# Performance work log

Measured on AMD Instinct MI355X. Metric: run time of the kernel, lower is better.

The kernel has to match this reference:

```python
import jax, jax.numpy as jnp
import numpy as np


def _layer_norm(x, w, b, eps=1e-5):
    mu = jnp.mean(x, axis=-1, keepdims=True)
    xc = x - mu
    var = jnp.mean(xc * xc, axis=-1, keepdims=True)
    return xc * jax.lax.rsqrt(var + eps) * w + b


def setup_inputs() -> dict:
    key = jax.random.key(0)
    ks = jax.random.split(key, 6)
    S, B, H = 2048, 2, 1024
    NH, NKV, HD = 16, 4, 64
    E, K, F = 8, 2, 4096
    w = lambda k, shape: 0.02 * jax.random.normal(k, shape, dtype=jnp.float32)
    return {
        "hidden_states": jax.random.normal(ks[0], (S, B, H), dtype=jnp.float32),
        "ln1_weight": jnp.ones((H,), jnp.float32),
        "ln1_bias": jnp.zeros((H,), jnp.float32),
        "ln2_weight": jnp.ones((H,), jnp.float32),
        "ln2_bias": jnp.zeros((H,), jnp.float32),
        "qkv_weight": w(ks[1], (H, (NH + 2 * NKV) * HD)),
        "proj_weight": w(ks[2], (H, H)),
        "router_weight": w(ks[3], (H, E)),
        "moe_w1": w(ks[4], (E, H, F)),
        "moe_w2": w(ks[5], (E, F, H)),
        "num_heads": NH,
        "num_kv_heads": NKV,
        "top_k": K,
    }


def reference(hidden_states, ln1_weight, ln1_bias, ln2_weight, ln2_bias,
              qkv_weight, proj_weight, router_weight, moe_w1, moe_w2,
              num_heads, num_kv_heads, top_k):
    S, B, H = hidden_states.shape
    HD = H // num_heads
    scale = 1.0 / (HD ** 0.5)

    # --- LN1 -> QKV projection (GQA split) ---
    ln1 = _layer_norm(hidden_states, ln1_weight, ln1_bias)
    qkv = ln1 @ qkv_weight                               # [S,B,(NH+2NKV)*HD]
    q_end = num_heads * HD
    k_end = q_end + num_kv_heads * HD
    q = qkv[..., :q_end].reshape(S, B, num_heads, HD)
    k = qkv[..., q_end:k_end].reshape(S, B, num_kv_heads, HD)
    v = qkv[..., k_end:].reshape(S, B, num_kv_heads, HD)
    rep = num_heads // num_kv_heads                      # repeat_interleave on head dim
    k = jnp.repeat(k, rep, axis=2)
    v = jnp.repeat(v, rep, axis=2)

    # --- causal SDPA, layout [B,NH,S,HD] ---
    q_bf = q.transpose(1, 2, 0, 3)
    k_bf = k.transpose(1, 2, 0, 3)
    v_bf = v.transpose(1, 2, 0, 3)
    scores = jnp.einsum('bhqd,bhkd->bhqk', q_bf, k_bf) * scale
    causal = jnp.tril(jnp.ones((S, S), dtype=bool))
    scores = jnp.where(causal, scores, jnp.finfo(scores.dtype).min)
    p = jax.nn.softmax(scores, axis=-1)
    attn = jnp.einsum('bhqk,bhkd->bhqd', p, v_bf)
    attn_out = attn.transpose(2, 0, 1, 3).reshape(S, B, H)  # back to [S,B,H]

    # --- output projection + residual ---
    h_attn = hidden_states + attn_out @ proj_weight

    # --- LN2 -> router top-k -> expert FFN -> weighted combine ---
    ln2 = _layer_norm(h_attn, ln2_weight, ln2_bias)
    T = S * B
    x = ln2.reshape(T, H)
    logits = x @ router_weight                           # [T,E]
    probs = jax.nn.softmax(logits, axis=-1)
    top_p, top_i = jax.lax.top_k(probs, top_k)           # [T,K]

    def expert_fn(_, w):
        w1, w2 = w
        return None, jax.nn.gelu(x @ w1, approximate=False) @ w2  # [T,H]

    _, outs = jax.lax.scan(expert_fn, None, (moe_w1, moe_w2))     # [E,T,H]
    gathered = outs[top_i, jnp.arange(T)[:, None], :]             # [T,K,H]
    moe_out = jnp.sum(gathered * top_p[..., None].astype(outs.dtype), axis=1)

    return h_attn + moe_out.reshape(S, B, H)
```

## Files before the change

### kernel.cpp

```cpp
#include <hip/hip_runtime.h>
#include <hip/hip_bf16.h>

constexpr int TT   = 4096;
constexpr int HH   = 1024;
constexpr int QKVN = 1536;
constexpr int FF   = 4096;

using f16x8  = __attribute__((ext_vector_type(8))) _Float16;
using f16x4  = __attribute__((ext_vector_type(4))) _Float16;
using bf16x8 = __attribute__((ext_vector_type(8))) short;
using s16x4  = __attribute__((ext_vector_type(4))) short;
using f32x4  = __attribute__((ext_vector_type(4))) float;

static __device__ __forceinline__ f32x4 mfma16(f16x8 a, f16x8 b, f32x4 c) {
  return __builtin_amdgcn_mfma_f32_16x16x32_f16(a, b, c, 0, 0, 0);
}
static __device__ __forceinline__ f32x4 mfmabf(bf16x8 a, bf16x8 b, f32x4 c) {
  return __builtin_amdgcn_mfma_f32_16x16x32_bf16(a, b, c, 0, 0, 0);
}
static __device__ __forceinline__ short f2bf(float f) {
  union { float f; unsigned u; } v; v.f = f;
  unsigned r = v.u + 0x7fffu + ((v.u >> 16) & 1u);
  return (short)(r >> 16);
}
static __device__ __forceinline__ void split16(float f, _Float16 &h, _Float16 &l) {
  _Float16 hh = (_Float16)f; h = hh; l = (_Float16)(f - (float)hh);
}
static __device__ __forceinline__ float fast_gelu(float x) {
  float u = 0.7978845608f * (x + 0.044715f * x * x * x);
  float a = __expf(-2.0f * fabsf(u));
  float t = (1.0f - a) * __builtin_amdgcn_rcpf(1.0f + a);
  t = copysignf(t, u);
  return 0.5f * x * (1.0f + t);
}
static __device__ __forceinline__ void gload16(const void* g, void* l) {
  __builtin_amdgcn_global_load_lds((__attribute__((address_space(1))) void*)(g),
                                   (__attribute__((address_space(3))) void*)(l), 16, 0, 0);
}

__global__ void zero_cnt(int* cnt) { if (threadIdx.x < 8) cnt[threadIdx.x] = 0; }

__global__ __launch_bounds__(256) void wconv_split(const float* __restrict__ W,
    _Float16* __restrict__ oh, _Float16* __restrict__ ol, int K, int N)
{
  __shared__ float ts[64][68];
  int n0 = blockIdx.x * 64, k0 = blockIdx.y * 64, t = threadIdx.x;
  #pragma unroll
  for (int it = 0; it < 4; it++) {
    int el = it * 1024 + t * 4; int r = el >> 6, c = el & 63;
    float4 v = *(const float4*)&W[(size_t)(k0 + r) * N + n0 + c];
    *(float4*)&ts[r][c] = v;
  }
  __syncthreads();
  #pragma unroll
  for (int it = 0; it < 4; it++) {
    int el = it * 1024 + t * 4; int nr = el >> 6, kc = el & 63;
    f16x4 hv, lv;
    #pragma unroll
    for (int q = 0; q < 4; q++) { _Float16 hh, ll; split16(ts[kc + q][nr], hh, ll); hv[q] = hh; lv[q] = ll; }
    size_t o = (size_t)(n0 + nr) * K + k0 + kc;
    *(f16x4*)&oh[o] = hv; *(f16x4*)&ol[o] = lv;
  }
}

__global__ __launch_bounds__(256) void wconv_bf(const float* __restrict__ W,
    short* __restrict__ o, int K, int N)
{
  __shared__ float ts[64][68];
  const float* Wz = W + (size_t)blockIdx.z * K * N;
  short* oz = o + (size_t)blockIdx.z * K * N;
  int n0 = blockIdx.x * 64, k0 = blockIdx.y * 64, t = threadIdx.x;
  #pragma unroll
  for (int it = 0; it < 4; it++) {
    int el = it * 1024 + t * 4; int r = el >> 6, c = el & 63;
    float4 v = *(const float4*)&Wz[(size_t)(k0 + r) * N + n0 + c];
    *(float4*)&ts[r][c] = v;
  }
  __syncthreads();
  #pragma unroll
  for (int it = 0; it < 4; it++) {
    int el = it * 1024 + t * 4; int nr = el >> 6, kc = el & 63;
    s16x4 bv;
    #pragma unroll
    for (int q = 0; q < 4; q++) bv[q] = f2bf(ts[kc + q][nr]);
    *(s16x4*)&oz[(size_t)(n0 + nr) * K + k0 + kc] = bv;
  }
}

__global__ __launch_bounds__(256) void vtrans(const float* __restrict__ qkv,
    _Float16* __restrict__ vh, _Float16* __restrict__ vl)
{
  __shared__ float ts[64][68];
  int bkv = blockIdx.x, b = bkv >> 2, kvh = bkv & 3;
  int s0 = blockIdx.y * 64, t = threadIdx.x;
  #pragma unroll
  for (int it = 0; it < 4; it++) {
    int el = it * 1024 + t * 4; int r = el >> 6, c = el & 63;
    float4 v = *(const float4*)&qkv[(size_t)((s0 + r) * 2 + b) * QKVN + 1280 + kvh * 64 + c];
    *(float4*)&ts[r][c] = v;
  }
  __syncthreads();
  #pragma unroll
  for (int it = 0; it < 4; it++) {
    int el = it * 1024 + t * 4; int d = el >> 6, sc = el & 63;
    f16x4 hv, lv;
    #pragma unroll
    for (int q = 0; q < 4; q++) { _Float16 hh, ll; split16(ts[sc + q][d], hh, ll); hv[q] = hh; lv[q] = ll; }
    size_t o = ((size_t)bkv * 64 + d) * 2048 + s0 + sc;
    *(f16x4*)&vh[o] = hv; *(f16x4*)&vl[o] = lv;
  }
}

template<int MODE>
__global__ __launch_bounds__(256) void ln_split(const float* __restrict__ in,
    const float* __restrict__ wt, const float* __restrict__ bs,
    _Float16* __restrict__ oh, _Float16* __restrict__ ol,
    float* __restrict__ xo, short* __restrict__ xbo)
{
  int row = blockIdx.x, tid = threadIdx.x;
  const float4* ip = (const float4*)(in + (size_t)row * HH);
  float4 v = ip[tid];
  float s = v.x + v.y + v.z + v.w;
  #pragma unroll
  for (int m = 1; m < 64; m <<= 1) s += __shfl_xor(s, m, 64);
  __shared__ float red1[4], red2[4];
  int wid = tid >> 6;
  if ((tid & 63) == 0) red1[wid] = s;
  __syncthreads();
  float mu = (red1[0] + red1[1] + red1[2] + red1[3]) * (1.0f / HH);
  float4 c; c.x = v.x - mu; c.y = v.y - mu; c.z = v.z - mu; c.w = v.w - mu;
  float s2 = c.x*c.x + c.y*c.y + c.z*c.z + c.w*c.w;
  #pragma unroll
  for (int m = 1; m < 64; m <<= 1) s2 += __shfl_xor(s2, m, 64);
  if ((tid & 63) == 0) red2[wid] = s2;
  __syncthreads();
  float ve = (red2[0] + red2[1] + red2[2] + red2[3]) * (1.0f / HH) + 1e-5f;
  float rs = rsqrtf(ve);
  rs = rs * (1.5f - 0.5f * ve * rs * rs);
  float4 wv = ((const float4*)wt)[tid], bv = ((const float4*)bs)[tid];
  float o4[4];
  o4[0] = c.x * rs * wv.x + bv.x; o4[1] = c.y * rs * wv.y + bv.y;
  o4[2] = c.z * rs * wv.z + bv.z; o4[3] = c.w * rs * wv.w + bv.w;
  size_t base = (size_t)row * HH + tid * 4;
  if (MODE == 0) {
    f16x4 hv, lv;
    #pragma unroll
    for (int q = 0; q < 4; q++) { _Float16 hh, ll; split16(o4[q], hh, ll); hv[q] = hh; lv[q] = ll; }
    *(f16x4*)&oh[base] = hv; *(f16x4*)&ol[base] = lv;
  } else {
    float4 ov; ov.x = o4[0]; ov.y = o4[1]; ov.z = o4[2]; ov.w = o4[3];
    *(float4*)&xo[base] = ov;
    s16x4 bvv;
    #pragma unroll
    for (int q = 0; q < 4; q++) bvv[q] = f2bf(o4[q]);
    *(s16x4*)&xbo[base] = bvv;
  }
}

template<int EPI>
__global__ __launch_bounds__(256) void gemm_split2(
    const _Float16* __restrict__ Agh, const _Float16* __restrict__ Agl,
    const _Float16* __restrict__ Bgh, const _Float16* __restrict__ Bgl,
    int K, float* __restrict__ C, int ldc, const float* __restrict__ resid,
    _Float16* __restrict__ kh, _Float16* __restrict__ kl)
{
  __shared__ _Float16 AhS[4096], AlS[4096], BhS[4096], BlS[4096];
  const int tid = threadIdx.x, lane = tid & 63, w = tid >> 6;
  const int wr = w >> 1, wc = w & 1;
  const int m0 = blockIdx.y * 128, n0 = blockIdx.x * 128;
  f32x4 acc[4][4] = {};
  const _Float16 *pah[2], *pal[2], *pbh[2], *pbl[2];
  int ldsb[2];
  #pragma unroll
  for (int i = 0; i < 2; i++) {
    int E = i * 2048 + w * 512 + lane * 8;
    int r = E >> 5, cc = E & 31;
    int cs = cc ^ ((r & 3) << 3);
    pah[i] = Agh + (size_t)(m0 + r) * K + cs;
    pal[i] = Agl + (size_t)(m0 + r) * K + cs;
    pbh[i] = Bgh + (size_t)(n0 + r) * K + cs;
    pbl[i] = Bgl + (size_t)(n0 + r) * K + cs;
    ldsb[i] = i * 2048 + w * 512;
  }
  const int rr = lane & 15, ko = (lane >> 4) * 8;
  const int xo = (rr & 3) << 3;
  for (int k0 = 0; k0 < K; k0 += 32) {
    __syncthreads();
    #pragma unroll
    for (int i = 0; i < 2; i++) {
      gload16(pah[i] + k0, &AhS[ldsb[i]]);
      gload16(pal[i] + k0, &AlS[ldsb[i]]);
      gload16(pbh[i] + k0, &BhS[ldsb[i]]);
      gload16(pbl[i] + k0, &BlS[ldsb[i]]);
    }
    __syncthreads();
    f16x8 fah[4], fal[4], fbh[4], fbl[4];
    #pragma unroll
    for (int m = 0; m < 4; m++) {
      int ro = (wr * 64 + m * 16 + rr) * 32 + (ko ^ xo);
      fah[m] = *(const f16x8*)&AhS[ro];
      fal[m] = *(const f16x8*)&AlS[ro];
    }
    #pragma unroll
    for (int n = 0; n < 4; n++) {
      int ro = (wc * 64 + n * 16 + rr) * 32 + (ko ^ xo);
      fbh[n] = *(const f16x8*)&BhS[ro];
      fbl[n] = *(const f16x8*)&BlS[ro];
    }
    #pragma unroll
    for (int m = 0; m < 4; m++)
      #pragma unroll
      for (int n = 0; n < 4; n++) {
        acc[m][n] = mfma16(fah[m], fbh[n], acc[m][n]);
        acc[m][n] = mfma16(fah[m], fbl[n], acc[m][n]);
        acc[m][n] = mfma16(fal[m], fbh[n], acc[m][n]);
      }
  }
  int r0 = m0 + wr * 64 + (lane >> 4) * 4;
  int c0 = n0 + wc * 64 + (lane & 15);
  #pragma unroll
  for (int m = 0; m < 4; m++)
    #pragma unroll
    for (int n = 0; n < 4; n++)
      #pragma unroll
      for (int j = 0; j < 4; j++) {
        int tr = r0 + m * 16 + j, tc = c0 + n * 16;
        size_t idx = (size_t)tr * ldc + tc;
        float v = acc[m][n][j];
        if (EPI == 1) v += resid[idx];
        C[idx] = v;
        if (EPI == 0 && tc >= 1024 && tc < 1280) {
          int s = tr >> 1, bb = tr & 1;
          int kvh = (tc - 1024) >> 6, d = (tc - 1024) & 63;
          _Float16 hh, ll; split16(v, hh, ll);
          size_t kidx = ((size_t)(bb * 4 + kvh) * 2048 + s) * 64 + d;
          kh[kidx] = hh; kl[kidx] = ll;
        }
      }
}

__global__ __launch_bounds__(256) void attn2(const float* __restrict__ qkv,
    const _Float16* __restrict__ khg, const _Float16* __restrict__ klg,
    const _Float16* __restrict__ vhg, const _Float16* __restrict__ vlg,
    _Float16* __restrict__ aoh, _Float16* __restrict__ aol)
{
  __shared__ _Float16 KhS[4096], KlS[4096], VhS[4096], VlS[4096];
  __shared__ _Float16 Ph[64][72], Pl[64][72];
  int bh = blockIdx.x;
  int qt = gridDim.y - 1 - blockIdx.y;
  int h = bh >> 1, b = bh & 1, kvh = h >> 2, bkv = b * 4 + kvh;
  int q0 = qt * 64;
  int tid = threadIdx.x, lane = tid & 63, w = tid >> 6;
  int rr = lane & 15, ko = (lane >> 4) * 8;
  const int xo8 = (rr & 7) << 3;
  int qrow = q0 + w * 16 + rr;
  const float* qp = qkv + (size_t)(qrow * 2 + b) * QKVN + h * 64;
  f16x8 qh[2], ql[2];
  #pragma unroll
  for (int kk = 0; kk < 2; kk++) {
    const float4* p = (const float4*)(qp + kk * 32 + ko);
    float4 v0 = p[0], v1 = p[1];
    float tq[8] = {v0.x, v0.y, v0.z, v0.w, v1.x, v1.y, v1.z, v1.w};
    f16x8 hv, lv;
    #pragma unroll
    for (int q = 0; q < 8; q++) { _Float16 hh, ll; split16(tq[q], hh, ll); hv[q] = hh; lv[q] = ll; }
    qh[kk] = hv; ql[kk] = lv;
  }
  const _Float16 *pk[2][2], *pv[2][2];
  int ldsb[2];
  #pragma unroll
  for (int i = 0; i < 2; i++) {
    int E = i * 2048 + w * 512 + lane * 8;
    int r = E >> 6, cc = E & 63;
    int cs = cc ^ ((r & 7) << 3);
    pk[i][0] = khg + ((size_t)bkv * 2048 + r) * 64 + cs;
    pk[i][1] = klg + ((size_t)bkv * 2048 + r) * 64 + cs;
    pv[i][0] = vhg + ((size_t)bkv * 64 + r) * 2048 + cs;
    pv[i][1] = vlg + ((size_t)bkv * 64 + r) * 2048 + cs;
    ldsb[i] = i * 2048 + w * 512;
  }
  f32x4 o[4] = {};
  float mo[4] = {-1e30f, -1e30f, -1e30f, -1e30f};
  float lo[4] = {0.f, 0.f, 0.f, 0.f};
  for (int ks = 0; ks <= q0; ks += 64) {
    __syncthreads();
    #pragma unroll
    for (int i = 0; i < 2; i++) {
      gload16(pk[i][0] + (size_t)ks * 64, &KhS[ldsb[i]]);
      gload16(pk[i][1] + (size_t)ks * 64, &KlS[ldsb[i]]);
      gload16(pv[i][0] + ks, &VhS[ldsb[i]]);
      gload16(pv[i][1] + ks, &VlS[ldsb[i]]);
    }
    __syncthreads();
    f32x4 s[4] = {};
    __builtin_amdgcn_s_setprio(1);
    #pragma unroll
    for (int n = 0; n < 4; n++)
      #pragma unroll
      for (int kk = 0; kk < 2; kk++) {
        int ro = (n * 16 + rr) * 64 + ((kk * 32 + ko) ^ xo8);
        f16x8 kbh = *(const f16x8*)&KhS[ro];
        f16x8 kbl = *(const f16x8*)&KlS[ro];
        s[n] = mfma16(qh[kk], kbh, s[n]);
        s[n] = mfma16(qh[kk], kbl, s[n]);
        s[n] = mfma16(ql[kk], kbh, s[n]);
      }
    __builtin_amdgcn_s_setprio(0);
    bool diag = (ks == q0);
    int myrow = q0 + w * 16 + (lane >> 4) * 4;
    #pragma unroll
    for (int n = 0; n < 4; n++)
      #pragma unroll
      for (int j = 0; j < 4; j++) {
        float v = s[n][j] * 0.125f;
        if (diag && (ks + n * 16 + rr) > (myrow + j)) v = -1e30f;
        s[n][j] = v;
      }
    float mt[4];
    #pragma unroll
    for (int j = 0; j < 4; j++) mt[j] = fmaxf(fmaxf(s[0][j], s[1][j]), fmaxf(s[2][j], s[3][j]));
    #pragma unroll
    for (int msk = 1; msk < 16; msk <<= 1)
      #pragma unroll
      for (int j = 0; j < 4; j++) mt[j] = fmaxf(mt[j], __shfl_xor(mt[j], msk, 64));
    float pvv[4][4], rsum[4];
    #pragma unroll
    for (int j = 0; j < 4; j++) {
      float mn = fmaxf(mo[j], mt[j]);
      float al = expf(mo[j] - mn);
      mo[j] = mn;
      rsum[j] = 0.f;
      #pragma unroll
      for (int n = 0; n < 4; n++) { float pp = expf(s[n][j] - mn); pvv[n][j] = pp; rsum[j] += pp; }
      lo[j] *= al;
      #pragma unroll
      for (int n = 0; n < 4; n++) o[n][j] *= al;
    }
    #pragma unroll
    for (int msk = 1; msk < 16; msk <<= 1)
      #pragma unroll
      for (int j = 0; j < 4; j++) rsum[j] += __shfl_xor(rsum[j], msk, 64);
    #pragma unroll
    for (int j = 0; j < 4; j++) lo[j] += rsum[j];
    int prow = w * 16 + (lane >> 4) * 4;
    #pragma unroll
    for (int n = 0; n < 4; n++)
      #pragma unroll
      for (int j = 0; j < 4; j++) {
        _Float16 hh, ll; split16(pvv[n][j], hh, ll);
        Ph[prow + j][n * 16 + rr] = hh;
        Pl[prow + j][n * 16 + rr] = ll;
      }
    __builtin_amdgcn_s_setprio(1);
    #pragma unroll
    for (int kk = 0; kk < 2; kk++) {
      f16x8 pah = *(const f16x8*)&Ph[w * 16 + rr][kk * 32 + ko];
      f16x8 pal = *(const f16x8*)&Pl[w * 16 + rr][kk * 32 + ko];
      #pragma unroll
      for (int dn = 0; dn < 4; dn++) {
        int ro = (dn * 16 + rr) * 64 + ((kk * 32 + ko) ^ xo8);
        f16x8 vbh = *(const f16x8*)&VhS[ro];
        f16x8 vbl = *(const f16x8*)&VlS[ro];
        o[dn] = mfma16(pah, vbh, o[dn]);
        o[dn] = mfma16(pah, vbl, o[dn]);
        o[dn] = mfma16(pal, vbh, o[dn]);
      }
    }
    __builtin_amdgcn_s_setprio(0);
  }
  float inv[4];
  #pragma unroll
  for (int j = 0; j < 4; j++) inv[j] = 1.0f / lo[j];
  int orow = q0 + w * 16 + (lane >> 4) * 4;
  int ocol = h * 64 + rr;
  #pragma unroll
  for (int dn = 0; dn < 4; dn++)
    #pragma unroll
    for (int j = 0; j < 4; j++) {
      float v = o[dn][j] * inv[j];
      _Float16 hh, ll; split16(v, hh, ll);
      size_t idx = (size_t)((orow + j) * 2 + b) * HH + ocol + dn * 16;
      aoh[idx] = hh; aol[idx] = ll;
    }
}

__global__ __launch_bounds__(256) void router_kernel(const float* __restrict__ x,
    const float* __restrict__ rw, int* __restrict__ list, float* __restrict__ listp,
    int* __restrict__ cnt)
{
  __shared__ float rws[HH * 8];
  int tid = threadIdx.x;
  for (int i = tid; i < HH * 8; i += 256) rws[i] = rw[i];
  __syncthreads();
  int t = blockIdx.x * 4 + (tid >> 6);
  int lane = tid & 63;
  const float* xp = x + (size_t)t * HH;
  float acc[8] = {};
  for (int i = lane; i < HH; i += 64) {
    float xv = xp[i];
    #pragma unroll
    for (int e = 0; e < 8; e++) acc[e] += xv * rws[i * 8 + e];
  }
  #pragma unroll
  for (int e = 0; e < 8; e++)
    #pragma unroll
    for (int m = 1; m < 64; m <<= 1) acc[e] += __shfl_xor(acc[e], m, 64);
  if (lane == 0) {
    float mx = acc[0];
    #pragma unroll
    for (int e = 1; e < 8; e++) mx = fmaxf(mx, acc[e]);
    float p[8], sum = 0.f;
    #pragma unroll
    for (int e = 0; e < 8; e++) { p[e] = expf(acc[e] - mx); sum += p[e]; }
    float inv = 1.0f / sum;
    int i1 = 0; float v1 = acc[0];
    #pragma unroll
    for (int e = 1; e < 8; e++) if (acc[e] > v1) { v1 = acc[e]; i1 = e; }
    int i2 = -1; float v2 = -3.4e38f;
    #pragma unroll
    for (int e = 0; e < 8; e++) if (e != i1 && acc[e] > v2) { v2 = acc[e]; i2 = e; }
    int pos1 = atomicAdd(&cnt[i1], 1);
    list[i1 * TT + pos1] = t; listp[i1 * TT + pos1] = p[i1] * inv;
    int pos2 = atomicAdd(&cnt[i2], 1);
    list[i2 * TT + pos2] = t; listp[i2 * TT + pos2] = p[i2] * inv;
  }
}

__global__ __launch_bounds__(256) void moe1_full(const short* __restrict__ xbf,
    const short* __restrict__ w1T, const int* __restrict__ list,
    const int* __restrict__ cnt, short* __restrict__ hidden)
{
  int e = blockIdx.z;
  int ce = cnt[e];
  int off = 0;
  #pragma unroll
  for (int i = 0; i < 8; i++) if (i < e) off += cnt[i];
  int m0 = blockIdx.y * 128;
  if (m0 >= ce) return;
  int n0 = blockIdx.x * 128;
  __shared__ short AS[8192], BS[8192];
  const int tid = threadIdx.x, lane = tid & 63, w = tid >> 6;
  const int wr = w >> 1, wc = w & 1;
  f32x4 acc[4][4] = {};
  const short *pa[4], *pb[4];
  int ldsb[4];
  #pragma unroll
  for (int i = 0; i < 4; i++) {
    int E = i * 2048 + w * 512 + lane * 8;
    int r = E >> 6, c = E & 63;
    int cs = c ^ ((r & 7) << 3);
    int apos = m0 + r; if (apos > ce - 1) apos = ce - 1;
    int tok = list[e * TT + apos];
    pa[i] = xbf + (size_t)tok * HH + cs;
    pb[i] = w1T + ((size_t)e * FF + n0 + r) * HH + cs;
    ldsb[i] = E;
  }
  const int rr = lane & 15, ko = (lane >> 4) * 8;
  const int xo = (rr & 7) << 3;
  for (int k0 = 0; k0 < HH; k0 += 64) {
    __syncthreads();
    #pragma unroll
    for (int i = 0; i < 4; i++) {
      gload16(pa[i] + k0, &AS[ldsb[i]]);
      gload16(pb[i] + k0, &BS[ldsb[i]]);
    }
    __syncthreads();
    #pragma unroll
    for (int kk = 0; kk < 2; kk++) {
      bf16x8 fa[4], fb[4];
      #pragma unroll
      for (int m = 0; m < 4; m++) fa[m] = *(const bf16x8*)&AS[(wr * 64 + m * 16 + rr) * 64 + ((kk * 32 + ko) ^ xo)];
      #pragma unroll
      for (int n = 0; n < 4; n++) fb[n] = *(const bf16x8*)&BS[(wc * 64 + n * 16 + rr) * 64 + ((kk * 32 + ko) ^ xo)];
      #pragma unroll
      for (int m = 0; m < 4; m++)
        #pragma unroll
        for (int n = 0; n < 4; n++) acc[m][n] = mfmabf(fa[m], fb[n], acc[m][n]);
    }
  }
  int p0 = m0 + wr * 64 + (lane >> 4) * 4;
  int c0 = n0 + wc * 64 + (lane & 15);
  #pragma unroll
  for (int m = 0; m < 4; m++)
    #pragma unroll
    for (int n = 0; n < 4; n++)
      #pragma unroll
      for (int j = 0; j < 4; j++) {
        int pos = p0 + m * 16 + j;
        if (pos < ce) {
          float v = fast_gelu(acc[m][n][j]);
          hidden[(size_t)(off + pos) * FF + c0 + n * 16] = f2bf(v);
        }
      }
}

__global__ __launch_bounds__(256) void moe2_full(const short* __restrict__ hidden,
    const short* __restrict__ w2T, const int* __restrict__ list,
    const float* __restrict__ listp, const int* __restrict__ cnt,
    float* __restrict__ outp)
{
  int e = blockIdx.z;
  int ce = cnt[e];
  int off = 0;
  #pragma unroll
  for (int i = 0; i < 8; i++) if (i < e) off += cnt[i];
  int m0 = blockIdx.y * 128;
  if (m0 >= ce) return;
  int n0 = blockIdx.x * 128;
  __shared__ short AS[8192], BS[8192];
  const int tid = threadIdx.x, lane = tid & 63, w = tid >> 6;
  const int wr = w >> 1, wc = w & 1;
  f32x4 acc[4][4] = {};
  const short *pa[4], *pb[4];
  int ldsb[4];
  #pragma unroll
  for (int i = 0; i < 4; i++) {
    int E = i * 2048 + w * 512 + lane * 8;
    int r = E >> 6, c = E & 63;
    int cs = c ^ ((r & 7) << 3);
    int apos = m0 + r; if (apos > ce - 1) apos = ce - 1;
    pa[i] = hidden + ((size_t)off + apos) * FF + cs;
    pb[i] = w2T + ((size_t)e * HH + n0 + r) * FF + cs;
    ldsb[i] = E;
  }
  const int rr = lane & 15, ko = (lane >> 4) * 8;
  const int xo = (rr & 7) << 3;
  for (int k0 = 0; k0 < FF; k0 += 64) {
    __syncthreads();
    #pragma unroll
    for (int i = 0; i < 4; i++) {
      gload16(pa[i] + k0, &AS[ldsb[i]]);
      gload16(pb[i] + k0, &BS[ldsb[i]]);
    }
    __syncthreads();
    #pragma unroll
    for (int kk = 0; kk < 2; kk++) {
      bf16x8 fa[4], fb[4];
      #pragma unroll
      for (int m = 0; m < 4; m++) fa[m] = *(const bf16x8*)&AS[(wr * 64 + m * 16 + rr) * 64 + ((kk * 32 + ko) ^ xo)];
      #pragma unroll
      for (int n = 0; n < 4; n++) fb[n] = *(const bf16x8*)&BS[(wc * 64 + n * 16 + rr) * 64 + ((kk * 32 + ko) ^ xo)];
      #pragma unroll
      for (int m = 0; m < 4; m++)
        #pragma unroll
        for (int n = 0; n < 4; n++) acc[m][n] = mfmabf(fa[m], fb[n], acc[m][n]);
    }
  }
  int p0 = m0 + wr * 64 + (lane >> 4) * 4;
  int c0 = n0 + wc * 64 + (lane & 15);
  #pragma unroll
  for (int m = 0; m < 4; m++)
    #pragma unroll
    for (int j = 0; j < 4; j++) {
      int pos = p0 + m * 16 + j;
      if (pos < ce) {
        int tk = list[e * TT + pos];
        float pw = listp[e * TT + pos];
        #pragma unroll
        for (int n = 0; n < 4; n++)
          atomicAdd(&outp[(size_t)tk * HH + c0 + n * 16], pw * acc[m][n][j]);
      }
    }
}

__global__ __launch_bounds__(256) void moe_gemm1(const float* __restrict__ x,
    const float* __restrict__ w1, const int* __restrict__ list,
    const int* __restrict__ cnt, short* __restrict__ hidden, int e)
{
  int ce = cnt[e];
  int m0 = blockIdx.y * 128;
  if (m0 >= ce) return;
  int n0 = blockIdx.x * 128;
  __shared__ short As[128][40], Bs[128][40];
  int tid = threadIdx.x, lane = tid & 63, w = tid >> 6, wr = w >> 1, wc = w & 1;
  f32x4 acc[4][4] = {};
  int arow = tid >> 1, akh = (tid & 1) * 16;
  int apos = m0 + arow;
  int tok = list[(size_t)e * TT + (apos < ce ? apos : 0)];
  const float* ap = x + (size_t)tok * HH + akh;
  int bn = tid & 127, bkh = (tid >> 7) * 16;
  const float* bp = w1 + (size_t)e * HH * FF + (size_t)bkh * FF + n0 + bn;
  for (int k0 = 0; k0 < HH; k0 += 32) {
    __syncthreads();
    {
      const float4* p = (const float4*)(ap + k0);
      bf16x8 s0, s1;
      #pragma unroll
      for (int q = 0; q < 2; q++) { float4 v = p[q]; s0[q*4] = f2bf(v.x); s0[q*4+1] = f2bf(v.y); s0[q*4+2] = f2bf(v.z); s0[q*4+3] = f2bf(v.w); }
      #pragma unroll
      for (int q = 0; q < 2; q++) { float4 v = p[q+2]; s1[q*4] = f2bf(v.x); s1[q*4+1] = f2bf(v.y); s1[q*4+2] = f2bf(v.z); s1[q*4+3] = f2bf(v.w); }
      *(bf16x8*)&As[arow][akh] = s0; *(bf16x8*)&As[arow][akh+8] = s1;
    }
    {
      const float* p = bp + (size_t)k0 * FF;
      bf16x8 s0, s1;
      #pragma unroll
      for (int q = 0; q < 8; q++) s0[q] = f2bf(p[(size_t)q * FF]);
      #pragma unroll
      for (int q = 0; q < 8; q++) s1[q] = f2bf(p[(size_t)(q+8) * FF]);
      *(bf16x8*)&Bs[bn][bkh] = s0; *(bf16x8*)&Bs[bn][bkh+8] = s1;
    }
    __syncthreads();
    int rr = lane & 15, ko = (lane >> 4) * 8;
    bf16x8 fa[4], fb[4];
    #pragma unroll
    for (int m = 0; m < 4; m++) fa[m] = *(bf16x8*)&As[wr*64 + m*16 + rr][ko];
    #pragma unroll
    for (int n = 0; n < 4; n++) fb[n] = *(bf16x8*)&Bs[wc*64 + n*16 + rr][ko];
    #pragma unroll
    for (int m = 0; m < 4; m++)
      #pragma unroll
      for (int n = 0; n < 4; n++) acc[m][n] = mfmabf(fa[m], fb[n], acc[m][n]);
  }
  int p0 = m0 + wr*64 + (lane >> 4) * 4;
  int c0 = n0 + wc*64 + (lane & 15);
  #pragma unroll
  for (int m = 0; m < 4; m++)
    #pragma unroll
    for (int n = 0; n < 4; n++)
      #pragma unroll
      for (int j = 0; j < 4; j++) {
        int pos = p0 + m*16 + j;
        if (pos < ce) {
          float v = acc[m][n][j];
          v = 0.5f * v * (1.0f + erff(v * 0.70710678f));
          hidden[(size_t)pos * FF + c0 + n*16] = f2bf(v);
        }
      }
}

__global__ __launch_bounds__(256) void moe_gemm2(const short* __restrict__ hidden,
    const float* __restrict__ w2, const int* __restrict__ list,
    const float* __restrict__ listp, const int* __restrict__ cnt,
    float* __restrict__ outp, int e)
{
  int ce = cnt[e];
  int m0 = blockIdx.y * 128;
  if (m0 >= ce) return;
  int n0 = blockIdx.x * 128;
  __shared__ short As[128][40], Bs[128][40];
  int tid = threadIdx.x, lane = tid & 63, w = tid >> 6, wr = w >> 1, wc = w & 1;
  f32x4 acc[4][4] = {};
  int arow = tid >> 1, akh = (tid & 1) * 16;
  int apos = m0 + arow;
  const short* ap = hidden + (size_t)(apos < ce ? apos : 0) * FF + akh;
  int bn = tid & 127, bkh = (tid >> 7) * 16;
  const float* bp = w2 + (size_t)e * FF * HH + (size_t)bkh * HH + n0 + bn;
  for (int k0 = 0; k0 < FF; k0 += 32) {
    __syncthreads();
    {
      const int4* p = (const int4*)(ap + k0);
      int4 a0 = p[0], a1 = p[1];
      *(int4*)&As[arow][akh]   = a0;
      *(int4*)&As[arow][akh+8] = a1;
    }
    {
      const float* p = bp + (size_t)k0 * HH;
      bf16x8 s0, s1;
      #pragma unroll
      for (int q = 0; q < 8; q++) s0[q] = f2bf(p[(size_t)q * HH]);
      #pragma unroll
      for (int q = 0; q < 8; q++) s1[q] = f2bf(p[(size_t)(q+8) * HH]);
      *(bf16x8*)&Bs[bn][bkh] = s0; *(bf16x8*)&Bs[bn][bkh+8] = s1;
    }
    __syncthreads();
    int rr = lane & 15, ko = (lane >> 4) * 8;
    bf16x8 fa[4], fb[4];
    #pragma unroll
    for (int m = 0; m < 4; m++) fa[m] = *(bf16x8*)&As[wr*64 + m*16 + rr][ko];
    #pragma unroll
    for (int n = 0; n < 4; n++) fb[n] = *(bf16x8*)&Bs[wc*64 + n*16 + rr][ko];
    #pragma unroll
    for (int m = 0; m < 4; m++)
      #pragma unroll
      for (int n = 0; n < 4; n++) acc[m][n] = mfmabf(fa[m], fb[n], acc[m][n]);
  }
  int p0 = m0 + wr*64 + (lane >> 4) * 4;
  int c0 = n0 + wc*64 + (lane & 15);
  #pragma unroll
  for (int m = 0; m < 4; m++)
    #pragma unroll
    for (int j = 0; j < 4; j++) {
      int pos = p0 + m*16 + j;
      if (pos < ce) {
        int tk = list[(size_t)e * TT + pos];
        float pw = listp[(size_t)e * TT + pos];
        #pragma unroll
        for (int n = 0; n < 4; n++)
          atomicAdd(&outp[(size_t)tk * HH + c0 + n*16], pw * acc[m][n][j]);
      }
    }
}

extern "C" void kernel_launch(void* const* d_in, const int* in_sizes, int n_in,
                              void* d_out, int out_size, void* d_ws, size_t ws_size,
                              hipStream_t stream)
{
  const float* hs      = (const float*)d_in[0];
  const float* ln1w    = (const float*)d_in[1];
  const float* ln1b    = (const float*)d_in[2];
  const float* ln2w    = (const float*)d_in[3];
  const float* ln2b    = (const float*)d_in[4];
  const float* qkvw    = (const float*)d_in[5];
  const float* projw   = (const float*)d_in[6];
  const float* routerw = (const float*)d_in[7];
  const float* w1      = (const float*)d_in[8];
  const float* w2      = (const float*)d_in[9];
  float* out = (float*)d_out;

  const size_t MB = 1024 * 1024;
  char* wsb = (char*)d_ws;
  bool full = ws_size >= 153 * MB;

  float*    qkvbuf = (float*)wsb;
  _Float16* khb    = (_Float16*)(wsb + 24 * MB);
  _Float16* klb    = (_Float16*)(wsb + 26 * MB);
  _Float16* vhb    = (_Float16*)(wsb + 28 * MB);
  _Float16* vlb    = (_Float16*)(wsb + 30 * MB);
  short*    hidden = (short*)wsb;
  size_t r2 = full ? 64 * MB : 32 * MB;
  _Float16* ln1h = (_Float16*)(wsb + r2);
  _Float16* ln1l = (_Float16*)(wsb + r2 + 8 * MB);
  _Float16* aohb = ln1h;
  _Float16* aolb = ln1l;
  float*    xbuf = (float*)(wsb + r2);
  short*    xbf  = (short*)(wsb + r2 + 16 * MB);
  size_t r3 = full ? 88 * MB : 56 * MB;
  _Float16* qkvwTh  = (_Float16*)(wsb + r3);
  _Float16* qkvwTl  = (_Float16*)(wsb + r3 + 3 * MB);
  _Float16* projwTh = (_Float16*)(wsb + r3 + 6 * MB);
  _Float16* projwTl = (_Float16*)(wsb + r3 + 8 * MB);
  short*    w1T     = (short*)(wsb + r3);
  short*    w2T     = (short*)(wsb + r3);
  size_t r4 = full ? 152 * MB : 66 * MB;
  int*   list  = (int*)(wsb + r4);
  float* listp = (float*)(wsb + r4 + 128 * 1024);
  int*   cnt   = (int*)(wsb + r4 + 256 * 1024);

  zero_cnt<<<1, 64, 0, stream>>>(cnt);
  wconv_split<<<dim3(QKVN / 64, HH / 64), 256, 0, stream>>>(qkvw, qkvwTh, qkvwTl, HH, QKVN);
  wconv_split<<<dim3(HH / 64, HH / 64), 256, 0, stream>>>(projw, projwTh, projwTl, HH, HH);
  ln_split<0><<<TT, 256, 0, stream>>>(hs, ln1w, ln1b, ln1h, ln1l, nullptr, nullptr);
  gemm_split2<0><<<dim3(QKVN / 128, TT / 128), 256, 0, stream>>>(
      ln1h, ln1l, qkvwTh, qkvwTl, HH, qkvbuf, QKVN, nullptr, khb, klb);
  vtrans<<<dim3(8, 32), 256, 0, stream>>>(qkvbuf, vhb, vlb);
  attn2<<<dim3(32, 32), 256, 0, stream>>>(qkvbuf, khb, klb, vhb, vlb, aohb, aolb);
  gemm_split2<1><<<dim3(HH / 128, TT / 128), 256, 0, stream>>>(
      aohb, aolb, projwTh, projwTl, HH, out, HH, hs, nullptr, nullptr);
  ln_split<1><<<TT, 256, 0, stream>>>(out, ln2w, ln2b, nullptr, nullptr, xbuf, xbf);
  router_kernel<<<TT / 4, 256, 0, stream>>>(xbuf, routerw, list, listp, cnt);
  if (full) {
    wconv_bf<<<dim3(FF / 64, HH / 64, 8), 256, 0, stream>>>(w1, w1T, HH, FF);
    moe1_full<<<dim3(FF / 128, TT / 128, 8), 256, 0, stream>>>(xbf, w1T, list, cnt, hidden);
    wconv_bf<<<dim3(HH / 64, FF / 64, 8), 256, 0, stream>>>(w2, w2T, FF, HH);
    moe2_full<<<dim3(HH / 128, TT / 128, 8), 256, 0, stream>>>(hidden, w2T, list, listp, cnt, out);
  } else {
    for (int e = 0; e < 8; e++) {
      moe_gemm1<<<dim3(FF / 128, TT / 128), 256, 0, stream>>>(xbuf, w1, list, cnt, hidden, e);
      moe_gemm2<<<dim3(HH / 128, TT / 128), 256, 0, stream>>>(hidden, w2, list, listp, cnt, out, e);
    }
  }
}
```

Before: 699.0 us.

## Interleave expert blocks in 1D grid and double-buffer LDS in MoE down-projection

Both MoE GEMM kernels now use a flat 1D grid with the expert index in the low bits. This interleaves blocks from different experts and pushes the early-exit check ahead of the offset computation, so work is spread more evenly across CUs. The second MoE GEMM also gains double-buffered LDS tiles: it prefetches the next K-slice while running MFMAs on the current one, with one barrier per iteration and s_setprio around the compute. This doubles LDS use for that kernel, which may reduce occupancy.

```diff
diff --git a/kernel.cpp b/kernel.cpp
--- a/kernel.cpp
+++ b/kernel.cpp
@@ -430,14 +430,17 @@
     const short* __restrict__ w1T, const int* __restrict__ list,
     const int* __restrict__ cnt, short* __restrict__ hidden)
 {
-  int e = blockIdx.z;
+  int id = blockIdx.x;
+  int e = id & 7;
+  int inner = id >> 3;
+  int mx = inner & 31, nx = inner >> 5;
   int ce = cnt[e];
+  int m0 = mx * 128;
+  if (m0 >= ce) return;
+  int n0 = nx * 128;
   int off = 0;
   #pragma unroll
   for (int i = 0; i < 8; i++) if (i < e) off += cnt[i];
-  int m0 = blockIdx.y * 128;
-  if (m0 >= ce) return;
-  int n0 = blockIdx.x * 128;
   __shared__ short AS[8192], BS[8192];
   const int tid = threadIdx.x, lane = tid & 63, w = tid >> 6;
   const int wr = w >> 1, wc = w & 1;
@@ -499,15 +502,18 @@
     const float* __restrict__ listp, const int* __restrict__ cnt,
     float* __restrict__ outp)
 {
-  int e = blockIdx.z;
+  int id = blockIdx.x;
+  int e = id & 7;
+  int inner = id >> 3;
+  int mx = inner & 31, nx = inner >> 5;
   int ce = cnt[e];
+  int m0 = mx * 128;
+  if (m0 >= ce) return;
+  int n0 = nx * 128;
   int off = 0;
   #pragma unroll
   for (int i = 0; i < 8; i++) if (i < e) off += cnt[i];
-  int m0 = blockIdx.y * 128;
-  if (m0 >= ce) return;
-  int n0 = blockIdx.x * 128;
-  __shared__ short AS[8192], BS[8192];
+  __shared__ short AS[2][8192], BS[2][8192];
   const int tid = threadIdx.x, lane = tid & 63, w = tid >> 6;
   const int wr = w >> 1, wc = w & 1;
   f32x4 acc[4][4] = {};
@@ -525,26 +531,38 @@
   }
   const int rr = lane & 15, ko = (lane >> 4) * 8;
   const int xo = (rr & 7) << 3;
+  #pragma unroll
+  for (int i = 0; i < 4; i++) {
+    gload16(pa[i], &AS[0][ldsb[i]]);
+    gload16(pb[i], &BS[0][ldsb[i]]);
+  }
+  __syncthreads();
+  int cb = 0;
   for (int k0 = 0; k0 < FF; k0 += 64) {
-    __syncthreads();
-    #pragma unroll
-    for (int i = 0; i < 4; i++) {
-      gload16(pa[i] + k0, &AS[ldsb[i]]);
-      gload16(pb[i] + k0, &BS[ldsb[i]]);
-    }
-    __syncthreads();
+    int nk = k0 + 64;
+    if (nk < FF) {
+      #pragma unroll
+      for (int i = 0; i < 4; i++) {
+        gload16(pa[i] + nk, &AS[cb ^ 1][ldsb[i]]);
+        gload16(pb[i] + nk, &BS[cb ^ 1][ldsb[i]]);
+      }
+    }
+    __builtin_amdgcn_s_setprio(1);
     #pragma unroll
     for (int kk = 0; kk < 2; kk++) {
       bf16x8 fa[4], fb[4];
       #pragma unroll
-      for (int m = 0; m < 4; m++) fa[m] = *(const bf16x8*)&AS[(wr * 64 + m * 16 + rr) * 64 + ((kk * 32 + ko) ^ xo)];
-      #pragma unroll
-      for (int n = 0; n < 4; n++) fb[n] = *(const bf16x8*)&BS[(wc * 64 + n * 16 + rr) * 64 + ((kk * 32 + ko) ^ xo)];
+      for (int m = 0; m < 4; m++) fa[m] = *(const bf16x8*)&AS[cb][(wr * 64 + m * 16 + rr) * 64 + ((kk * 32 + ko) ^ xo)];
+      #pragma unroll
+      for (int n = 0; n < 4; n++) fb[n] = *(const bf16x8*)&BS[cb][(wc * 64 + n * 16 + rr) * 64 + ((kk * 32 + ko) ^ xo)];
       #pragma unroll
       for (int m = 0; m < 4; m++)
         #pragma unroll
         for (int n = 0; n < 4; n++) acc[m][n] = mfmabf(fa[m], fb[n], acc[m][n]);
     }
+    __builtin_amdgcn_s_setprio(0);
+    __syncthreads();
+    cb ^= 1;
   }
   int p0 = m0 + wr * 64 + (lane >> 4) * 4;
   int c0 = n0 + wc * 64 + (lane & 15);
@@ -751,9 +769,9 @@
   router_kernel<<<TT / 4, 256, 0, stream>>>(xbuf, routerw, list, listp, cnt);
   if (full) {
     wconv_bf<<<dim3(FF / 64, HH / 64, 8), 256, 0, stream>>>(w1, w1T, HH, FF);
-    moe1_full<<<dim3(FF / 128, TT / 128, 8), 256, 0, stream>>>(xbf, w1T, list, cnt, hidden);
+    moe1_full<<<8 * 32 * 32, 256, 0, stream>>>(xbf, w1T, list, cnt, hidden);
     wconv_bf<<<dim3(HH / 64, FF / 64, 8), 256, 0, stream>>>(w2, w2T, FF, HH);
-    moe2_full<<<dim3(HH / 128, TT / 128, 8), 256, 0, stream>>>(hidden, w2T, list, listp, cnt, out);
+    moe2_full<<<8 * 32 * 8, 256, 0, stream>>>(hidden, w2T, list, listp, cnt, out);
   } else {
     for (int e = 0; e < 8; e++) {
       moe_gemm1<<<dim3(FF / 128, TT / 128), 256, 0, stream>>>(xbuf, w1, list, cnt, hidden, e);
```

Result: no change. 690.7 us (-1.2%).
